# Kernel tuning notes

Hardware: AMD Instinct MI355X
Metric: run time of the kernel (lower is better)

## Reference

```python
import jax, jax.numpy as jnp
import numpy as np

EPS = 0.0  # init_eps=0, learn_eps=False -> fixed buffer
N_NODES = 50000
N_EDGES = 800000
D_NODE = 128
D_EDGE = 64


def setup_inputs() -> dict:
    key = jax.random.key(0)
    ks = jax.random.split(key, 10)
    s = lambda fan: 1.0 / np.sqrt(fan)
    return {
        "node_feat": jax.random.normal(ks[0], (N_NODES, D_NODE), jnp.float32),
        "edge_feat": jax.random.normal(ks[1], (N_EDGES, D_EDGE), jnp.float32),
        "W0": jax.random.normal(ks[2], (D_EDGE, D_EDGE), jnp.float32) * s(D_EDGE),
        "b0": jax.random.normal(ks[3], (D_EDGE,), jnp.float32) * s(D_EDGE),
        "W1": jax.random.normal(ks[4], (D_EDGE, D_NODE), jnp.float32) * s(D_EDGE),
        "b1": jax.random.normal(ks[5], (D_NODE,), jnp.float32) * s(D_EDGE),
        "Wa": jax.random.normal(ks[6], (D_NODE, D_NODE), jnp.float32) * s(D_NODE),
        "ba": jax.random.normal(ks[7], (D_NODE,), jnp.float32) * s(D_NODE),
        "src": jax.random.randint(ks[8], (N_EDGES,), 0, N_NODES, jnp.int64),
        "dst": jax.random.randint(ks[9], (N_EDGES,), 0, N_NODES, jnp.int64),
    }


def reference(node_feat, edge_feat, W0, b0, W1, b1, Wa, ba, src, dst):
    # edge transform MLP: relu(Linear) -> relu(Linear)  [E, D_NODE]
    e = jax.nn.relu(edge_feat @ W0 + b0)
    e = jax.nn.relu(e @ W1 + b1)
    # per-edge message: relu(x_src + e)  [E, D_NODE]
    m = jax.nn.relu(node_feat[src] + e)
    # scatter-sum to destination nodes  [N, D_NODE]
    neigh = jax.ops.segment_sum(m, dst, num_segments=node_feat.shape[0])
    rst = (1.0 + EPS) * node_feat + neigh
    # apply_func: Linear(128, 128)
    return rst @ Wa + ba
```

## Files before the change

### kernel.cpp

```cpp
#include <hip/hip_runtime.h>

typedef short bf16x8 __attribute__((ext_vector_type(8)));
typedef float f32x4 __attribute__((ext_vector_type(4)));
typedef unsigned short u16x2 __attribute__((ext_vector_type(2)));
typedef unsigned short u16x4 __attribute__((ext_vector_type(4)));
typedef unsigned short u16x8 __attribute__((ext_vector_type(8)));

static constexpr int N_NODES = 50000;
static constexpr int N_EDGES = 800000;
static constexpr int D_NODE = 128;
static constexpr int D_EDGE = 64;

static constexpr size_t START_OFF = 0;
static constexpr size_t FILL_OFF  = 262144;
static constexpr size_t PERM_OFF  = 524288;
static constexpr size_t SRCP_OFF  = PERM_OFF + (size_t)N_EDGES * 4;
static constexpr size_t DSTP_OFF  = SRCP_OFF + (size_t)N_EDGES * 4;
static constexpr size_t NF16_OFF  = DSTP_OFF + (size_t)N_EDGES * 4;
static constexpr size_t WS_NEED   = NF16_OFF + (size_t)N_NODES * D_NODE * 2;

__device__ __forceinline__ unsigned short f2bf(float f) {
    union { float f; unsigned u; } v; v.f = f;
    return (unsigned short)((v.u + 0x7fffu + ((v.u >> 16) & 1u)) >> 16);
}
__device__ __forceinline__ float bf2f(unsigned short h) {
    union { unsigned u; float f; } v; v.u = ((unsigned)h) << 16;
    return v.f;
}

__global__ void kz(int* __restrict__ a, int n) {
    int i = blockIdx.x * blockDim.x + threadIdx.x;
    if (i < n) a[i] = 0;
}

__global__ void kh(const int* __restrict__ dst, int* __restrict__ start) {
    int e = blockIdx.x * blockDim.x + threadIdx.x;
    if (e < N_EDGES) atomicAdd(&start[dst[e] + 1], 1);
}

__global__ __launch_bounds__(256) void ks1(const int* __restrict__ a, int* __restrict__ bsum, int n) {
    __shared__ int sd[256];
    const int t = threadIdx.x;
    int i = blockIdx.x * 256 + t;
    sd[t] = (i < n) ? a[i] : 0;
    __syncthreads();
    for (int off = 128; off > 0; off >>= 1) {
        if (t < off) sd[t] += sd[t + off];
        __syncthreads();
    }
    if (t == 0) bsum[blockIdx.x] = sd[0];
}

__global__ __launch_bounds__(256) void ks2(int* __restrict__ bsum, int nb) {
    __shared__ int sd[256];
    const int t = threadIdx.x;
    sd[t] = (t < nb) ? bsum[t] : 0;
    __syncthreads();
    for (int off = 1; off < 256; off <<= 1) {
        int v = (t >= off) ? sd[t - off] : 0;
        __syncthreads();
        sd[t] += v;
        __syncthreads();
    }
    if (t < nb) bsum[t] = sd[t];
}

__global__ __launch_bounds__(256) void ks3(const int* __restrict__ bsum,
                                           int* __restrict__ start, int* __restrict__ fill, int n) {
    __shared__ int sd[256];
    const int t = threadIdx.x;
    const int i = blockIdx.x * 256 + t;
    sd[t] = (i < n) ? start[i] : 0;
    __syncthreads();
    for (int off = 1; off < 256; off <<= 1) {
        int v = (t >= off) ? sd[t - off] : 0;
        __syncthreads();
        sd[t] += v;
        __syncthreads();
    }
    const int off0 = (blockIdx.x > 0) ? bsum[blockIdx.x - 1] : 0;
    const int val = sd[t] + off0;
    if (i < n) start[i] = val;
    if (i < N_NODES) fill[i] = val;
}

__global__ void kpos(const int* __restrict__ dst, const int* __restrict__ src,
                     int* __restrict__ fill, int* __restrict__ perm,
                     int* __restrict__ srcp, int* __restrict__ dstp) {
    int e = blockIdx.x * blockDim.x + threadIdx.x;
    if (e < N_EDGES) {
        int d = dst[e];
        int p = atomicAdd(&fill[d], 1);
        perm[p] = e;
        srcp[p] = src[e];
        dstp[p] = d;
    }
}

__global__ __launch_bounds__(256) void k_prep(const float* __restrict__ nf,
                                              float* __restrict__ out,
                                              unsigned short* __restrict__ nf16t) {
    const int tid = threadIdx.x;
    const int lm = tid & 15;
    const int node = blockIdx.x * 16 + (tid >> 4);
    if (node >= N_NODES) return;
    const float* nrow = nf + (size_t)node * D_NODE;
    float* orow = out + (size_t)node * D_NODE;
    f32x4 y0 = *(const f32x4*)(nrow + lm * 8);
    f32x4 y1 = *(const f32x4*)(nrow + lm * 8 + 4);
    *(f32x4*)(orow + lm * 8) = y0;
    *(f32x4*)(orow + lm * 8 + 4) = y1;
    u16x8 tv;
#pragma unroll
    for (int nt = 0; nt < 8; ++nt) tv[nt] = f2bf(nrow[nt * 16 + lm]);
    *(u16x8*)(nf16t + (size_t)node * D_NODE + lm * 8) = tv;
}

__global__ __launch_bounds__(256) void k_edge_fused(
    const float* __restrict__ ef, const unsigned short* __restrict__ nf16t,
    const float* __restrict__ W0, const float* __restrict__ b0,
    const float* __restrict__ W1, const float* __restrict__ b1,
    const int* __restrict__ perm, const int* __restrict__ srcp,
    const int* __restrict__ dstp, float* __restrict__ out)
{
    __shared__ unsigned short w0f[2 * 4 * 64 * 8];
    __shared__ unsigned short w1f[2 * 8 * 64 * 8];
    __shared__ __align__(16) unsigned short hT[4][16][72];
    __shared__ __align__(16) unsigned short mT[4][16][136];

    const int tid = threadIdx.x;
    for (int f = tid; f < 4096; f += 256) {
        int j = f & 7, lane = (f >> 3) & 63, nt = (f >> 9) & 3, ks = (f >> 11) & 1;
        int k = ks * 32 + ((lane >> 4) << 2) + (j & 3) + ((j & 4) << 2);
        int n = nt * 16 + (lane & 15);
        w0f[f] = f2bf(W0[k * 64 + n]);
    }
    for (int f = tid; f < 8192; f += 256) {
        int j = f & 7, lane = (f >> 3) & 63, nt = (f >> 9) & 7, ks = (f >> 12) & 1;
        int k = ks * 32 + ((lane >> 4) << 2) + (j & 3) + ((j & 4) << 2);
        int n = nt * 16 + (lane & 15);
        w1f[f] = f2bf(W1[k * 128 + n]);
    }
    __syncthreads();

    const int wv = tid >> 6;
    const int lane = tid & 63;
    const int lm = lane & 15;
    const int lq = lane >> 4;

    float b0r[4], b1r[8];
#pragma unroll
    for (int nt = 0; nt < 4; ++nt) b0r[nt] = b0[nt * 16 + lm];
#pragma unroll
    for (int nt = 0; nt < 8; ++nt) b1r[nt] = b1[nt * 16 + lm];

    const bf16x8* w0v = (const bf16x8*)w0f;
    const bf16x8* w1v = (const bf16x8*)w1f;

    const int wtile0 = (blockIdx.x * 4 + wv) * 4;

    for (int t = 0; t < 4; ++t) {
        const int ebase = (wtile0 + t) * 16;

        const int e_m = perm[ebase + lm];
        const int s_m = srcp[ebase + lm];
        const int d_m = dstp[ebase + lm];

        const f32x4* er = (const f32x4*)(ef + (size_t)e_m * D_EDGE);
        f32x4 a0 = er[lq];
        f32x4 a1 = er[4 + lq];
        f32x4 a2 = er[8 + lq];
        f32x4 a3 = er[12 + lq];

        u16x8 ngb[4];
#pragma unroll
        for (int r = 0; r < 4; ++r) {
            const int s_row = __shfl(s_m, lq * 4 + r);
            ngb[r] = *(const u16x8*)(nf16t + (size_t)s_row * D_NODE + lm * 8);
        }

        bf16x8 af0, af1;
#pragma unroll
        for (int j = 0; j < 4; ++j) {
            af0[j] = (short)f2bf(a0[j]); af0[j + 4] = (short)f2bf(a1[j]);
            af1[j] = (short)f2bf(a2[j]); af1[j + 4] = (short)f2bf(a3[j]);
        }

        f32x4 h[4];
#pragma unroll
        for (int nt = 0; nt < 4; ++nt) h[nt] = f32x4{0.f, 0.f, 0.f, 0.f};
#pragma unroll
        for (int nt = 0; nt < 4; ++nt) {
            h[nt] = __builtin_amdgcn_mfma_f32_16x16x32_bf16(af0, w0v[(0 * 4 + nt) * 64 + lane], h[nt], 0, 0, 0);
            h[nt] = __builtin_amdgcn_mfma_f32_16x16x32_bf16(af1, w0v[(1 * 4 + nt) * 64 + lane], h[nt], 0, 0, 0);
        }
#pragma unroll
        for (int nt = 0; nt < 4; ++nt)
#pragma unroll
            for (int r = 0; r < 4; ++r) {
                float x = h[nt][r] + b0r[nt];
                hT[wv][lq * 4 + r][nt * 16 + lm] = f2bf(fmaxf(x, 0.f));
            }

        const unsigned short* hrow = &hT[wv][lm][0];
        u16x4 p0 = *(const u16x4*)(hrow + lq * 4);
        u16x4 p1 = *(const u16x4*)(hrow + 16 + lq * 4);
        u16x4 p2 = *(const u16x4*)(hrow + 32 + lq * 4);
        u16x4 p3 = *(const u16x4*)(hrow + 48 + lq * 4);
        bf16x8 g0, g1;
#pragma unroll
        for (int j = 0; j < 4; ++j) {
            g0[j] = (short)p0[j]; g0[j + 4] = (short)p1[j];
            g1[j] = (short)p2[j]; g1[j + 4] = (short)p3[j];
        }

        f32x4 o[8];
#pragma unroll
        for (int nt = 0; nt < 8; ++nt) o[nt] = f32x4{0.f, 0.f, 0.f, 0.f};
#pragma unroll
        for (int nt = 0; nt < 8; ++nt) {
            o[nt] = __builtin_amdgcn_mfma_f32_16x16x32_bf16(g0, w1v[(0 * 8 + nt) * 64 + lane], o[nt], 0, 0, 0);
            o[nt] = __builtin_amdgcn_mfma_f32_16x16x32_bf16(g1, w1v[(1 * 8 + nt) * 64 + lane], o[nt], 0, 0, 0);
        }

#pragma unroll
        for (int r = 0; r < 4; ++r)
#pragma unroll
            for (int nt = 0; nt < 8; ++nt) {
                float e2 = fmaxf(o[nt][r] + b1r[nt], 0.f);
                float x = e2 + bf2f(ngb[r][nt]);
                mT[wv][lq * 4 + r][nt * 16 + lm] = f2bf(fmaxf(x, 0.f));
            }

        asm volatile("" ::: "memory");
        __syncthreads();

        float acc0 = 0.f, acc1 = 0.f;
        int dprev = __shfl(d_m, 0);
#pragma unroll
        for (int r = 0; r < 16; ++r) {
            const int dr = __shfl(d_m, r);
            if (dr != dprev) {
                float* orow = out + (size_t)dprev * D_NODE + lane * 2;
                unsafeAtomicAdd(orow, acc0);
                unsafeAtomicAdd(orow + 1, acc1);
                acc0 = 0.f; acc1 = 0.f; dprev = dr;
            }
            const u16x2 v = *(const u16x2*)&mT[wv][r][lane * 2];
            acc0 += bf2f(v[0]);
            acc1 += bf2f(v[1]);
        }
        float* orow = out + (size_t)dprev * D_NODE + lane * 2;
        unsafeAtomicAdd(orow, acc0);
        unsafeAtomicAdd(orow + 1, acc1);

        asm volatile("" ::: "memory");
    }
}

__global__ void k_copy(const f32x4* __restrict__ s, f32x4* __restrict__ d, int n4) {
    int stride = gridDim.x * blockDim.x;
    for (int i = blockIdx.x * blockDim.x + threadIdx.x; i < n4; i += stride)
        d[i] = s[i];
}

__global__ __launch_bounds__(256) void k_edge(
    const float* __restrict__ ef, const float* __restrict__ nf,
    const float* __restrict__ W0, const float* __restrict__ b0,
    const float* __restrict__ W1, const float* __restrict__ b1,
    const int* __restrict__ src, const int* __restrict__ dst,
    float* __restrict__ acc)
{
    __shared__ unsigned short w0f[2 * 4 * 64 * 8];
    __shared__ unsigned short w1f[2 * 8 * 64 * 8];
    __shared__ unsigned short hT[4][16][72];

    const int tid = threadIdx.x;
    for (int f = tid; f < 4096; f += 256) {
        int j = f & 7, lane = (f >> 3) & 63, nt = (f >> 9) & 3, ks = (f >> 11) & 1;
        int k = ks * 32 + ((lane >> 4) << 2) + (j & 3) + ((j & 4) << 2);
        int n = nt * 16 + (lane & 15);
        w0f[f] = f2bf(W0[k * 64 + n]);
    }
    for (int f = tid; f < 8192; f += 256) {
        int j = f & 7, lane = (f >> 3) & 63, nt = (f >> 9) & 7, ks = (f >> 12) & 1;
        int k = ks * 32 + ((lane >> 4) << 2) + (j & 3) + ((j & 4) << 2);
        int n = nt * 16 + (lane & 15);
        w1f[f] = f2bf(W1[k * 128 + n]);
    }
    __syncthreads();

    const int wv = tid >> 6;
    const int lane = tid & 63;
    const int lm = lane & 15;
    const int lq = lane >> 4;

    float b0r[4], b1r[8];
#pragma unroll
    for (int nt = 0; nt < 4; ++nt) b0r[nt] = b0[nt * 16 + lm];
#pragma unroll
    for (int nt = 0; nt < 8; ++nt) b1r[nt] = b1[nt * 16 + lm];

    const bf16x8* w0v = (const bf16x8*)w0f;
    const bf16x8* w1v = (const bf16x8*)w1f;

    for (int t = 0; t < 4; ++t) {
        const int tile = (blockIdx.x * 4 + wv) * 4 + t;
        const int ebase = tile * 16;

        const f32x4* er = (const f32x4*)(ef + (size_t)(ebase + lm) * D_EDGE);
        f32x4 a0 = er[lq];
        f32x4 a1 = er[4 + lq];
        f32x4 a2 = er[8 + lq];
        f32x4 a3 = er[12 + lq];
        bf16x8 af0, af1;
#pragma unroll
        for (int j = 0; j < 4; ++j) {
            af0[j] = (short)f2bf(a0[j]); af0[j + 4] = (short)f2bf(a1[j]);
            af1[j] = (short)f2bf(a2[j]); af1[j + 4] = (short)f2bf(a3[j]);
        }

        f32x4 h[4];
#pragma unroll
        for (int nt = 0; nt < 4; ++nt) h[nt] = f32x4{0.f, 0.f, 0.f, 0.f};
#pragma unroll
        for (int nt = 0; nt < 4; ++nt) {
            h[nt] = __builtin_amdgcn_mfma_f32_16x16x32_bf16(af0, w0v[(0 * 4 + nt) * 64 + lane], h[nt], 0, 0, 0);
            h[nt] = __builtin_amdgcn_mfma_f32_16x16x32_bf16(af1, w0v[(1 * 4 + nt) * 64 + lane], h[nt], 0, 0, 0);
        }
#pragma unroll
        for (int nt = 0; nt < 4; ++nt)
#pragma unroll
            for (int r = 0; r < 4; ++r) {
                float x = h[nt][r] + b0r[nt];
                hT[wv][lq * 4 + r][nt * 16 + lm] = f2bf(fmaxf(x, 0.f));
            }

        const unsigned short* hrow = &hT[wv][lm][0];
        u16x4 p0 = *(const u16x4*)(hrow + lq * 4);
        u16x4 p1 = *(const u16x4*)(hrow + 16 + lq * 4);
        u16x4 p2 = *(const u16x4*)(hrow + 32 + lq * 4);
        u16x4 p3 = *(const u16x4*)(hrow + 48 + lq * 4);
        bf16x8 g0, g1;
#pragma unroll
        for (int j = 0; j < 4; ++j) {
            g0[j] = (short)p0[j]; g0[j + 4] = (short)p1[j];
            g1[j] = (short)p2[j]; g1[j + 4] = (short)p3[j];
        }

        f32x4 o[8];
#pragma unroll
        for (int nt = 0; nt < 8; ++nt) o[nt] = f32x4{0.f, 0.f, 0.f, 0.f};
#pragma unroll
        for (int nt = 0; nt < 8; ++nt) {
            o[nt] = __builtin_amdgcn_mfma_f32_16x16x32_bf16(g0, w1v[(0 * 8 + nt) * 64 + lane], o[nt], 0, 0, 0);
            o[nt] = __builtin_amdgcn_mfma_f32_16x16x32_bf16(g1, w1v[(1 * 8 + nt) * 64 + lane], o[nt], 0, 0, 0);
        }

        const int e0 = ebase + lq * 4;
        int s_[4], d_[4];
#pragma unroll
        for (int r = 0; r < 4; ++r) { s_[r] = src[e0 + r]; d_[r] = dst[e0 + r]; }
#pragma unroll
        for (int r = 0; r < 4; ++r) {
            const float* nrow = nf + (size_t)s_[r] * D_NODE;
            float* arow = acc + (size_t)d_[r] * D_NODE;
#pragma unroll
            for (int nt = 0; nt < 8; ++nt) {
                float e2 = fmaxf(o[nt][r] + b1r[nt], 0.f);
                float x = e2 + nrow[nt * 16 + lm];
                unsafeAtomicAdd(&arow[nt * 16 + lm], fmaxf(x, 0.f));
            }
        }
    }
}

__global__ __launch_bounds__(256) void k_out(
    const float* __restrict__ Wa, const float* __restrict__ ba,
    float* __restrict__ out)
{
    __shared__ unsigned short waf[4 * 8 * 64 * 8];

    const int tid = threadIdx.x;
    for (int f = tid; f < 16384; f += 256) {
        int j = f & 7, lane = (f >> 3) & 63, nt = (f >> 9) & 7, ks = (f >> 12) & 3;
        int k = ks * 32 + ((lane >> 4) << 2) + (j & 3) + ((j & 4) << 2);
        int n = nt * 16 + (lane & 15);
        waf[f] = f2bf(Wa[k * 128 + n]);
    }
    __syncthreads();

    const int wv = tid >> 6;
    const int lane = tid & 63;
    const int lm = lane & 15;
    const int lq = lane >> 4;

    const int tile = blockIdx.x * 4 + wv;
    if (tile >= N_NODES / 16) return;
    const int rbase = tile * 16;

    const f32x4* arow = (const f32x4*)(out + (size_t)(rbase + lm) * D_NODE);
    const bf16x8* wav = (const bf16x8*)waf;

    bf16x8 afr[4];
#pragma unroll
    for (int ks = 0; ks < 4; ++ks) {
        f32x4 y0 = arow[ks * 8 + lq];
        f32x4 y1 = arow[ks * 8 + 4 + lq];
#pragma unroll
        for (int j = 0; j < 4; ++j) {
            afr[ks][j] = (short)f2bf(y0[j]);
            afr[ks][j + 4] = (short)f2bf(y1[j]);
        }
    }

    float bar[8];
#pragma unroll
    for (int nt = 0; nt < 8; ++nt) bar[nt] = ba[nt * 16 + lm];

    f32x4 o[8];
#pragma unroll
    for (int nt = 0; nt < 8; ++nt) o[nt] = f32x4{0.f, 0.f, 0.f, 0.f};
#pragma unroll
    for (int ks = 0; ks < 4; ++ks)
#pragma unroll
        for (int nt = 0; nt < 8; ++nt)
            o[nt] = __builtin_amdgcn_mfma_f32_16x16x32_bf16(afr[ks], wav[(ks * 8 + nt) * 64 + lane], o[nt], 0, 0, 0);

#pragma unroll
    for (int nt = 0; nt < 8; ++nt)
#pragma unroll
        for (int r = 0; r < 4; ++r)
            out[(size_t)(rbase + lq * 4 + r) * D_NODE + nt * 16 + lm] = o[nt][r] + bar[nt];
}

extern "C" void kernel_launch(void* const* d_in, const int* in_sizes, int n_in,
                              void* d_out, int out_size, void* d_ws, size_t ws_size,
                              hipStream_t stream) {
    const float* nf = (const float*)d_in[0];
    const float* ef = (const float*)d_in[1];
    const float* W0 = (const float*)d_in[2];
    const float* b0 = (const float*)d_in[3];
    const float* W1 = (const float*)d_in[4];
    const float* b1 = (const float*)d_in[5];
    const float* Wa = (const float*)d_in[6];
    const float* ba = (const float*)d_in[7];
    const int* src = (const int*)d_in[8];
    const int* dst = (const int*)d_in[9];
    float* out = (float*)d_out;

    if (ws_size >= WS_NEED) {
        char* ws = (char*)d_ws;
        int* start = (int*)(ws + START_OFF);
        int* fill  = (int*)(ws + FILL_OFF);
        int* perm  = (int*)(ws + PERM_OFF);
        int* srcp  = (int*)(ws + SRCP_OFF);
        int* dstp  = (int*)(ws + DSTP_OFF);
        unsigned short* nf16t = (unsigned short*)(ws + NF16_OFF);
        int* bsum  = perm;

        const int n_scan = N_NODES + 1;
        const int nb = (n_scan + 255) / 256;

        k_prep<<<(N_NODES + 15) / 16, 256, 0, stream>>>(nf, out, nf16t);

        kz<<<(n_scan + 255) / 256, 256, 0, stream>>>(start, n_scan);
        kh<<<(N_EDGES + 255) / 256, 256, 0, stream>>>(dst, start);
        ks1<<<nb, 256, 0, stream>>>(start, bsum, n_scan);
        ks2<<<1, 256, 0, stream>>>(bsum, nb);
        ks3<<<nb, 256, 0, stream>>>(bsum, start, fill, n_scan);
        kpos<<<(N_EDGES + 255) / 256, 256, 0, stream>>>(dst, src, fill, perm, srcp, dstp);

        k_edge_fused<<<N_EDGES / (16 * 4 * 4), 256, 0, stream>>>(
            ef, nf16t, W0, b0, W1, b1, perm, srcp, dstp, out);
    } else {
        k_copy<<<2048, 256, 0, stream>>>((const f32x4*)nf, (f32x4*)out, N_NODES * D_NODE / 4);
        k_edge<<<N_EDGES / (16 * 4 * 4), 256, 0, stream>>>(ef, nf, W0, b0, W1, b1, src, dst, out);
    }

    k_out<<<(N_NODES / 16 + 3) / 4, 256, 0, stream>>>(Wa, ba, out);
}
```

Measured before the change: 276.9 us.

## Segment-reduce edge messages in registers via cross-lane shuffles instead of LDS

Replaces the LDS staging of per-edge messages (bf16 round-trip plus a block-wide barrier) with an in-register run-length reduction over destination nodes. Partial sums are combined with xor shuffles and then emitted as atomics. It also adds a minimum-occupancy hint to the launch bounds. This drops the shared-memory buffer, the bf16 quantization and the __syncthreads, at the cost of extra shuffles on each destination change and more register pressure under the occupancy constraint.

Measured after the change: 414.5 us. 1.5x slower.

```diff
diff --git a/kernel.cpp b/kernel.cpp
--- a/kernel.cpp
+++ b/kernel.cpp
@@ -2,7 +2,6 @@
 
 typedef short bf16x8 __attribute__((ext_vector_type(8)));
 typedef float f32x4 __attribute__((ext_vector_type(4)));
-typedef unsigned short u16x2 __attribute__((ext_vector_type(2)));
 typedef unsigned short u16x4 __attribute__((ext_vector_type(4)));
 typedef unsigned short u16x8 __attribute__((ext_vector_type(8)));
 
@@ -116,7 +115,7 @@
     *(u16x8*)(nf16t + (size_t)node * D_NODE + lm * 8) = tv;
 }
 
-__global__ __launch_bounds__(256) void k_edge_fused(
+__global__ __launch_bounds__(256, 4) void k_edge_fused(
     const float* __restrict__ ef, const unsigned short* __restrict__ nf16t,
     const float* __restrict__ W0, const float* __restrict__ b0,
     const float* __restrict__ W1, const float* __restrict__ b1,
@@ -126,7 +125,6 @@
     __shared__ unsigned short w0f[2 * 4 * 64 * 8];
     __shared__ unsigned short w1f[2 * 8 * 64 * 8];
     __shared__ __align__(16) unsigned short hT[4][16][72];
-    __shared__ __align__(16) unsigned short mT[4][16][136];
 
     const int tid = threadIdx.x;
     for (int f = tid; f < 4096; f += 256) {
@@ -224,37 +222,53 @@
         }
 
 #pragma unroll
-        for (int r = 0; r < 4; ++r)
+        for (int nt = 0; nt < 8; ++nt)
+#pragma unroll
+            for (int r = 0; r < 4; ++r) {
+                float e2 = fmaxf(o[nt][r] + b1r[nt], 0.f);
+                o[nt][r] = fmaxf(e2 + bf2f(ngb[r][nt]), 0.f);
+            }
+
+        float acc[8];
+#pragma unroll
+        for (int nt = 0; nt < 8; ++nt) acc[nt] = 0.f;
+        int dcur = __builtin_amdgcn_readlane(d_m, 0);
+
+#pragma unroll
+        for (int i = 0; i < 16; ++i) {
+            const int di = __builtin_amdgcn_readlane(d_m, i);
+            if (di != dcur) {
+#pragma unroll
+                for (int nt = 0; nt < 8; ++nt) {
+                    acc[nt] += __shfl_xor(acc[nt], 16);
+                    acc[nt] += __shfl_xor(acc[nt], 32);
+                }
+                float v0 = (lq & 2) ? ((lq & 1) ? acc[6] : acc[4]) : ((lq & 1) ? acc[2] : acc[0]);
+                float v1 = (lq & 2) ? ((lq & 1) ? acc[7] : acc[5]) : ((lq & 1) ? acc[3] : acc[1]);
+                float* orow = out + (size_t)dcur * D_NODE + lq * 32 + lm;
+                unsafeAtomicAdd(orow, v0);
+                unsafeAtomicAdd(orow + 16, v1);
+#pragma unroll
+                for (int nt = 0; nt < 8; ++nt) acc[nt] = 0.f;
+                dcur = di;
+            }
+            if (lq == (i >> 2)) {
+#pragma unroll
+                for (int nt = 0; nt < 8; ++nt) acc[nt] += o[nt][i & 3];
+            }
+        }
+        {
 #pragma unroll
             for (int nt = 0; nt < 8; ++nt) {
-                float e2 = fmaxf(o[nt][r] + b1r[nt], 0.f);
-                float x = e2 + bf2f(ngb[r][nt]);
-                mT[wv][lq * 4 + r][nt * 16 + lm] = f2bf(fmaxf(x, 0.f));
-            }
-
-        asm volatile("" ::: "memory");
-        __syncthreads();
-
-        float acc0 = 0.f, acc1 = 0.f;
-        int dprev = __shfl(d_m, 0);
-#pragma unroll
-        for (int r = 0; r < 16; ++r) {
-            const int dr = __shfl(d_m, r);
-            if (dr != dprev) {
-                float* orow = out + (size_t)dprev * D_NODE + lane * 2;
-                unsafeAtomicAdd(orow, acc0);
-                unsafeAtomicAdd(orow + 1, acc1);
-                acc0 = 0.f; acc1 = 0.f; dprev = dr;
-            }
-            const u16x2 v = *(const u16x2*)&mT[wv][r][lane * 2];
-            acc0 += bf2f(v[0]);
-            acc1 += bf2f(v[1]);
-        }
-        float* orow = out + (size_t)dprev * D_NODE + lane * 2;
-        unsafeAtomicAdd(orow, acc0);
-        unsafeAtomicAdd(orow + 1, acc1);
-
-        asm volatile("" ::: "memory");
+                acc[nt] += __shfl_xor(acc[nt], 16);
+                acc[nt] += __shfl_xor(acc[nt], 32);
+            }
+            float v0 = (lq & 2) ? ((lq & 1) ? acc[6] : acc[4]) : ((lq & 1) ? acc[2] : acc[0]);
+            float v1 = (lq & 2) ? ((lq & 1) ? acc[7] : acc[5]) : ((lq & 1) ? acc[3] : acc[1]);
+            float* orow = out + (size_t)dcur * D_NODE + lq * 32 + lm;
+            unsafeAtomicAdd(orow, v0);
+            unsafeAtomicAdd(orow + 16, v1);
+        }
     }
 }
 
```

## Pack edge metadata into int4, remap blocks per XCD, drop block barrier

Applied to the files above, without the earlier changes.

Per-edge permutation, source and destination indices are packed into one int4 array, so the fused edge kernel issues a single 16-byte load instead of three separate loads. Block IDs are remapped so contiguous sorted-edge ranges land on the same XCD, which aims at better L2 locality for the atomics on destination rows. The block-wide __syncthreads before the per-wave scatter is replaced with an LDS waitcnt plus a scheduling barrier, since each wave reads only its own mT slice. The epilogue loop order is also swapped. The packed layout adds a padding word per edge and uses more workspace memory.

Result: no change. 280.1 us (+1.1%).

```diff
diff --git a/kernel.cpp b/kernel.cpp
--- a/kernel.cpp
+++ b/kernel.cpp
@@ -13,10 +13,8 @@
 
 static constexpr size_t START_OFF = 0;
 static constexpr size_t FILL_OFF  = 262144;
-static constexpr size_t PERM_OFF  = 524288;
-static constexpr size_t SRCP_OFF  = PERM_OFF + (size_t)N_EDGES * 4;
-static constexpr size_t DSTP_OFF  = SRCP_OFF + (size_t)N_EDGES * 4;
-static constexpr size_t NF16_OFF  = DSTP_OFF + (size_t)N_EDGES * 4;
+static constexpr size_t META_OFF  = 524288;
+static constexpr size_t NF16_OFF  = META_OFF + (size_t)N_EDGES * 16;
 static constexpr size_t WS_NEED   = NF16_OFF + (size_t)N_NODES * D_NODE * 2;
 
 __device__ __forceinline__ unsigned short f2bf(float f) {
@@ -85,15 +83,12 @@
 }
 
 __global__ void kpos(const int* __restrict__ dst, const int* __restrict__ src,
-                     int* __restrict__ fill, int* __restrict__ perm,
-                     int* __restrict__ srcp, int* __restrict__ dstp) {
+                     int* __restrict__ fill, int4* __restrict__ meta) {
     int e = blockIdx.x * blockDim.x + threadIdx.x;
     if (e < N_EDGES) {
         int d = dst[e];
         int p = atomicAdd(&fill[d], 1);
-        perm[p] = e;
-        srcp[p] = src[e];
-        dstp[p] = d;
+        meta[p] = int4{e, src[e], d, 0};
     }
 }
 
@@ -116,12 +111,11 @@
     *(u16x8*)(nf16t + (size_t)node * D_NODE + lm * 8) = tv;
 }
 
-__global__ __launch_bounds__(256) void k_edge_fused(
+__global__ __launch_bounds__(256) void k_fused(
     const float* __restrict__ ef, const unsigned short* __restrict__ nf16t,
     const float* __restrict__ W0, const float* __restrict__ b0,
     const float* __restrict__ W1, const float* __restrict__ b1,
-    const int* __restrict__ perm, const int* __restrict__ srcp,
-    const int* __restrict__ dstp, float* __restrict__ out)
+    const int4* __restrict__ meta, float* __restrict__ out)
 {
     __shared__ unsigned short w0f[2 * 4 * 64 * 8];
     __shared__ unsigned short w1f[2 * 8 * 64 * 8];
@@ -143,6 +137,14 @@
     }
     __syncthreads();
 
+    int bid = blockIdx.x;
+    {
+        const int nwg = gridDim.x;
+        const int q = nwg >> 3, rr = nwg & 7;
+        const int xcd = bid & 7, j = bid >> 3;
+        bid = (xcd < rr ? xcd * (q + 1) : rr * (q + 1) + (xcd - rr) * q) + j;
+    }
+
     const int wv = tid >> 6;
     const int lane = tid & 63;
     const int lm = lane & 15;
@@ -157,14 +159,13 @@
     const bf16x8* w0v = (const bf16x8*)w0f;
     const bf16x8* w1v = (const bf16x8*)w1f;
 
-    const int wtile0 = (blockIdx.x * 4 + wv) * 4;
+    const int wtile0 = (bid * 4 + wv) * 4;
 
     for (int t = 0; t < 4; ++t) {
         const int ebase = (wtile0 + t) * 16;
 
-        const int e_m = perm[ebase + lm];
-        const int s_m = srcp[ebase + lm];
-        const int d_m = dstp[ebase + lm];
+        const int4 m4 = meta[ebase + lm];
+        const int e_m = m4.x, s_m = m4.y, d_m = m4.z;
 
         const f32x4* er = (const f32x4*)(ef + (size_t)e_m * D_EDGE);
         f32x4 a0 = er[lq];
@@ -224,16 +225,16 @@
         }
 
 #pragma unroll
-        for (int r = 0; r < 4; ++r)
-#pragma unroll
-            for (int nt = 0; nt < 8; ++nt) {
+        for (int nt = 0; nt < 8; ++nt)
+#pragma unroll
+            for (int r = 0; r < 4; ++r) {
                 float e2 = fmaxf(o[nt][r] + b1r[nt], 0.f);
                 float x = e2 + bf2f(ngb[r][nt]);
                 mT[wv][lq * 4 + r][nt * 16 + lm] = f2bf(fmaxf(x, 0.f));
             }
 
-        asm volatile("" ::: "memory");
-        __syncthreads();
+        asm volatile("s_waitcnt lgkmcnt(0)" ::: "memory");
+        __builtin_amdgcn_sched_barrier(0);
 
         float acc0 = 0.f, acc1 = 0.f;
         int dprev = __shfl(d_m, 0);
@@ -453,11 +454,9 @@
         char* ws = (char*)d_ws;
         int* start = (int*)(ws + START_OFF);
         int* fill  = (int*)(ws + FILL_OFF);
-        int* perm  = (int*)(ws + PERM_OFF);
-        int* srcp  = (int*)(ws + SRCP_OFF);
-        int* dstp  = (int*)(ws + DSTP_OFF);
+        int4* meta = (int4*)(ws + META_OFF);
         unsigned short* nf16t = (unsigned short*)(ws + NF16_OFF);
-        int* bsum  = perm;
+        int* bsum  = (int*)(ws + META_OFF);
 
         const int n_scan = N_NODES + 1;
         const int nb = (n_scan + 255) / 256;
@@ -469,10 +468,10 @@
         ks1<<<nb, 256, 0, stream>>>(start, bsum, n_scan);
         ks2<<<1, 256, 0, stream>>>(bsum, nb);
         ks3<<<nb, 256, 0, stream>>>(bsum, start, fill, n_scan);
-        kpos<<<(N_EDGES + 255) / 256, 256, 0, stream>>>(dst, src, fill, perm, srcp, dstp);
-
-        k_edge_fused<<<N_EDGES / (16 * 4 * 4), 256, 0, stream>>>(
-            ef, nf16t, W0, b0, W1, b1, perm, srcp, dstp, out);
+        kpos<<<(N_EDGES + 255) / 256, 256, 0, stream>>>(dst, src, fill, meta);
+
+        k_fused<<<N_EDGES / 256, 256, 0, stream>>>(
+            ef, nf16t, W0, b0, W1, b1, meta, out);
     } else {
         k_copy<<<2048, 256, 0, stream>>>((const f32x4*)nf, (f32x4*)out, N_NODES * D_NODE / 4);
         k_edge<<<N_EDGES / (16 * 4 * 4), 256, 0, stream>>>(ef, nf, W0, b0, W1, b1, src, dst, out);
```
